# Kernel optimization log

Hardware: AMD Instinct MI355X
Metric: run time of the kernel (lower is better)

The kernel has to match this reference:

```python
import jax, jax.numpy as jnp
import numpy as np

N, IN, HID, OUT, C, H = 50000, 1488, 1024, 512, 32, 8
E = 800000

def setup_inputs() -> dict:
    key = jax.random.key(0)
    ks = jax.random.split(key, 16)
    s = lambda k, shape, fan: jax.random.normal(k, shape, jnp.float32) * (1.0 / np.sqrt(fan))
    return {
        "x": jax.random.normal(ks[0], (N, IN), jnp.float32),
        "edge_index": jax.random.randint(ks[1], (2, E), 0, N, jnp.int64),
        "ln_g": jnp.ones((IN,), jnp.float32),
        "ln_b": jnp.zeros((IN,), jnp.float32),
        "W1": s(ks[2], (IN, HID), IN), "b1": jnp.zeros((HID,), jnp.float32),
        "W2": s(ks[3], (HID, OUT), HID), "b2": jnp.zeros((OUT,), jnp.float32),
        "Wr": s(ks[4], (OUT, C * H), OUT), "br": jnp.zeros((C * H,), jnp.float32),
        "Wg": s(ks[5], (OUT, C * H), OUT),
        "att_src": s(ks[6], (H, C), C),
        "att_dst": s(ks[7], (H, C), C),
        "bg": jnp.zeros((C * H,), jnp.float32),
    }

def reference(x, edge_index, ln_g, ln_b, W1, b1, W2, b2, Wr, br, Wg, att_src, att_dst, bg):
    n = x.shape[0]
    # LayerNorm
    mu = jnp.mean(x, axis=-1, keepdims=True)
    var = jnp.mean(jnp.square(x - mu), axis=-1, keepdims=True)
    xn = (x - mu) * jax.lax.rsqrt(var + 1e-5) * ln_g + ln_b
    # init_proj MLP
    h = jax.nn.relu(xn @ W1 + b1) @ W2 + b2            # [N, OUT]
    res = h @ Wr + br                                   # [N, H*C]
    # GATConv (add_self_loops=True, dropout inactive in eval)
    loops = jnp.arange(n, dtype=edge_index.dtype)
    src = jnp.concatenate([edge_index[0], loops])
    dst = jnp.concatenate([edge_index[1], loops])
    g = (h @ Wg).reshape(n, H, C)                       # [N, H, C]
    a_src = jnp.sum(g * att_src, axis=-1)               # [N, H]
    a_dst = jnp.sum(g * att_dst, axis=-1)               # [N, H]
    e = jax.nn.leaky_relu(a_src[src] + a_dst[dst], 0.2) # [E', H]
    m = jax.ops.segment_max(e, dst, num_segments=n)     # per-dst softmax (stable)
    ex = jnp.exp(e - m[dst])
    denom = jax.ops.segment_sum(ex, dst, num_segments=n)
    alpha = ex / (denom[dst] + 1e-16)                   # [E', H]
    msg = alpha[:, :, None] * g[src]                    # [E', H, C]
    agg = jax.ops.segment_sum(msg, dst, num_segments=n) # [N, H, C]
    out = agg.reshape(n, H * C) + bg
    return jax.nn.elu(out) + res
```

## Files before the change

kernel.cpp:

```cpp
#include <hip/hip_runtime.h>
#include <hip/hip_bf16.h>
#include <cstdint>
#include <cstddef>

#define NND 50000
#define DIN 1488
#define DINP 1536
#define DHID 1024
#define DOUT 512
#define DHC 256
#define NE 800000
#define NHD 8
#define SPLITC 256

typedef __attribute__((ext_vector_type(8))) short short8;
typedef __attribute__((ext_vector_type(4))) short short4v;
typedef __attribute__((ext_vector_type(4))) float f32x4;
typedef __attribute__((ext_vector_type(4))) int int4v;
typedef unsigned short ushort_t;

__device__ __forceinline__ unsigned short f2bf(float f){
  union { float f; unsigned u; } v; v.f = f;
  unsigned r = v.u + 0x7fffu + ((v.u >> 16) & 1u);
  return (unsigned short)(r >> 16);
}
__device__ __forceinline__ float bf2f(unsigned short u){
  union { unsigned u; float f; } v; v.u = ((unsigned)u) << 16;
  return v.f;
}

__device__ __forceinline__ void async16(const void* g, void* l){
  __builtin_amdgcn_global_load_lds((__attribute__((address_space(1))) void*)g,
                                   (__attribute__((address_space(3))) void*)l, 16, 0, 0);
}

__device__ __forceinline__ void tc_tile(const float* __restrict__ W,
                                        ushort_t* __restrict__ WT,
                                        int K, int Nn, int Kp, int bx, int by){
  __shared__ float tile[32][33];
  const int tx = threadIdx.x & 31, ty = threadIdx.x >> 5;
  const int k0 = bx*32, n0 = by*32;
  for (int i = ty; i < 32; i += 8){
    int k = k0 + i, n = n0 + tx;
    tile[i][tx] = (k < K && n < Nn) ? W[(size_t)k*Nn + n] : 0.f;
  }
  __syncthreads();
  for (int i = ty; i < 32; i += 8){
    int n = n0 + i, k = k0 + tx;
    if (n < Nn && k < Kp) WT[(size_t)n*Kp + k] = f2bf(tile[tx][i]);
  }
}
__global__ __launch_bounds__(256) void prep_kernel(const float* W1, const float* W2,
                                                   const float* Wr, const float* Wg,
                                                   ushort_t* W1T, ushort_t* W2T,
                                                   ushort_t* WrgT, int* cnt){
  int b = blockIdx.x;
  if (b < 1536){ tc_tile(W1, W1T, DIN, DHID, DINP, b % 48, b / 48); return; }
  b -= 1536;
  if (b < 512){ tc_tile(W2, W2T, DHID, DOUT, DHID, b % 32, b / 32); return; }
  b -= 512;
  if (b < 128){ tc_tile(Wr, WrgT, DOUT, DHC, DOUT, b % 16, b / 16); return; }
  b -= 128;
  if (b < 128){ tc_tile(Wg, WrgT + 256*DOUT, DOUT, DHC, DOUT, b % 16, b / 16); return; }
  b -= 128;
  { int i = b*256 + threadIdx.x; if (i < NND) cnt[i] = 0; }
}

#define LN_BLOCKS 12500
__global__ __launch_bounds__(256) void ln_count(const float* __restrict__ x,
                                                const float* __restrict__ gw,
                                                const float* __restrict__ bw,
                                                ushort_t* __restrict__ xn,
                                                const int* __restrict__ ei,
                                                int* __restrict__ cnt){
  const int bid = blockIdx.x;
  if (bid >= LN_BLOCKS){
    int e = (bid - LN_BLOCKS)*256 + threadIdx.x;
    if (e < NE) atomicAdd(&cnt[ei[NE + e]], 1);
    return;
  }
  const int wid = threadIdx.x >> 6, lane = threadIdx.x & 63;
  const int row = bid*4 + wid;
  if (row >= NND) return;
  const float* xr = x + (size_t)row * DIN;
  float s = 0.f, sq = 0.f;
  for (int i = lane*4; i < DIN; i += 256){
    f32x4 v = *(const f32x4*)(xr + i);
    s  += v.x + v.y + v.z + v.w;
    sq += v.x*v.x + v.y*v.y + v.z*v.z + v.w*v.w;
  }
  #pragma unroll
  for (int o = 32; o; o >>= 1){ s += __shfl_xor(s, o); sq += __shfl_xor(sq, o); }
  const float mu = s * (1.f/DIN);
  const float var = sq * (1.f/DIN) - mu*mu;
  const float rstd = rsqrtf(var + 1e-5f);
  ushort_t* xo = xn + (size_t)row * DINP;
  for (int i = lane*4; i < DIN; i += 256){
    f32x4 v = *(const f32x4*)(xr + i);
    f32x4 gg = *(const f32x4*)(gw + i);
    f32x4 bb = *(const f32x4*)(bw + i);
    union { ushort_t u[4]; unsigned long long q; } o;
    o.u[0] = f2bf((v.x-mu)*rstd*gg.x + bb.x);
    o.u[1] = f2bf((v.y-mu)*rstd*gg.y + bb.y);
    o.u[2] = f2bf((v.z-mu)*rstd*gg.z + bb.z);
    o.u[3] = f2bf((v.w-mu)*rstd*gg.w + bb.w);
    *(unsigned long long*)(xo + i) = o.q;
  }
  if (lane < (DINP - DIN)) xo[DIN + lane] = 0;
}

#define G1_NWG 3128
template<int ACT, int MODE, int CB>
__global__ __launch_bounds__(256, 2) void gemm128(const ushort_t* __restrict__ A,
                                                  const ushort_t* __restrict__ BT,
                                                  const float* __restrict__ bias,
                                                  void* __restrict__ out0,
                                                  void* __restrict__ out1,
                                                  int M, int Nn, int K,
                                                  const int* __restrict__ cnt,
                                                  int* __restrict__ offs,
                                                  int* __restrict__ cur){
  __shared__ __align__(16) ushort_t lds[2][2][128*64];
  const int t = threadIdx.x, wid = t >> 6, lane = t & 63;

  if (blockIdx.x == 0){
    int* buf = (int*)&lds[0][0][0];
    const int chunk = (NND + 255) >> 8;
    const int s0 = t*chunk;
    const int s1 = (s0 + chunk < NND) ? s0 + chunk : NND;
    int s = 0;
    for (int i = s0; i < s1; i += 4){
      int4v v = *(const int4v*)(cnt + i);
      s += v.x + v.y + v.z + v.w + 4;
    }
    buf[t] = s; __syncthreads();
    for (int o = 1; o < 256; o <<= 1){
      int xv = (t >= o) ? buf[t-o] : 0;
      __syncthreads();
      buf[t] += xv;
      __syncthreads();
    }
    int run = buf[t] - s;
    for (int i = s0; i < s1; i += 4){
      int4v v = *(const int4v*)(cnt + i);
      int4v cu;
      cu.x = run; run += v.x + 1;
      cu.y = run; run += v.y + 1;
      cu.z = run; run += v.z + 1;
      cu.w = run; run += v.w + 1;
      *(int4v*)(cur + i)  = cu;
      *(int4v*)(offs + i) = cu;
    }
    if (t == 255) offs[NND] = run;
    return;
  }

  const int bid = blockIdx.x - 1, nwg = G1_NWG;
  const int q = nwg >> 3, r = nwg & 7;
  const int xcd = bid & 7, slot = bid >> 3;
  const int lg = (xcd < r ? xcd*(q+1) : r*(q+1) + (xcd - r)*q) + slot;
  const int brow = (lg / CB) * 128, bcol = (lg % CB) * 128;

  const int l8  = t >> 3;
  const int cb  = (t & 7) << 4;
  const int scb = cb ^ ((l8 & 7) << 4);
  const ushort_t* pAr[4]; const ushort_t* pBr[4];
  #pragma unroll
  for (int rd = 0; rd < 4; ++rd){
    int ra = brow + rd*32 + l8; ra = ra < M ? ra : M-1;
    int rb = bcol + rd*32 + l8; rb = rb < Nn ? rb : Nn-1;
    pAr[rd] = A  + (size_t)ra*K + (scb >> 1);
    pBr[rd] = BT + (size_t)rb*K + (scb >> 1);
  }
  const int w8 = wid * 8;

#define STAGE1(buf, kt) do {                                           \
    const int _o = (kt) * 64;                                          \
    _Pragma("unroll")                                                  \
    for (int _rd = 0; _rd < 4; ++_rd){                                 \
      async16(pAr[_rd] + _o, &lds[buf][0][(_rd*32 + w8)*64]);          \
      async16(pBr[_rd] + _o, &lds[buf][1][(_rd*32 + w8)*64]);          \
    }                                                                  \
  } while(0)

  f32x4 acc[4][4];
  #pragma unroll
  for (int i=0;i<4;i++)
    #pragma unroll
    for (int j=0;j<4;j++) acc[i][j] = (f32x4){0.f,0.f,0.f,0.f};

  const int wr = (wid >> 1)*64, wc = (wid & 1)*64;
  const int fr = lane & 15;
  const int kb0 = (lane >> 4) << 4;
  const int sx  = (fr & 7) << 4;
  const int ko0 = ((kb0      ) ^ sx) >> 1;
  const int ko1 = ((kb0 | 64 ) ^ sx) >> 1;

  const int nk = K >> 6;
  STAGE1(0, 0);
  STAGE1(1, 1);
  for (int kt = 0; kt < nk; ++kt){
    const ushort_t* bA = lds[kt & 1][0];
    const ushort_t* bB = lds[kt & 1][1];
    if (kt + 1 < nk) asm volatile("s_waitcnt vmcnt(8)" ::: "memory");
    else             asm volatile("s_waitcnt vmcnt(0)" ::: "memory");
    __builtin_amdgcn_s_barrier();
    short8 af[4][2], bf_[4][2];
    #pragma unroll
    for (int m=0;m<4;m++){
      const int ra = (wr + m*16 + fr)*64;
      const int rb = (wc + m*16 + fr)*64;
      af[m][0]  = *(const short8*)&bA[ra + ko0];
      af[m][1]  = *(const short8*)&bA[ra + ko1];
      bf_[m][0] = *(const short8*)&bB[rb + ko0];
      bf_[m][1] = *(const short8*)&bB[rb + ko1];
    }
    asm volatile("s_waitcnt lgkmcnt(0)" ::: "memory");
    __builtin_amdgcn_sched_barrier(0);
    __builtin_amdgcn_s_barrier();
    if (kt + 2 < nk) STAGE1(kt & 1, kt + 2);
    __builtin_amdgcn_s_setprio(1);
    #pragma unroll
    for (int m=0;m<4;m++)
      #pragma unroll
      for (int n=0;n<4;n++){
        acc[m][n] = __builtin_amdgcn_mfma_f32_16x16x32_bf16(af[m][0], bf_[n][0], acc[m][n], 0, 0, 0);
        acc[m][n] = __builtin_amdgcn_mfma_f32_16x16x32_bf16(af[m][1], bf_[n][1], acc[m][n], 0, 0, 0);
      }
    __builtin_amdgcn_s_setprio(0);
  }
#undef STAGE1

  bool isf32;
  float* outF = nullptr; ushort_t* outB = nullptr; int ostride = 0, ocb = 0;
  if (MODE == 0){ isf32 = true;  outF = (float*)out0;    ostride = Nn; ocb = bcol; }
  else if (MODE == 1){ isf32 = false; outB = (ushort_t*)out0; ostride = Nn; ocb = bcol; }
  else {
    if (bcol < SPLITC){ isf32 = true;  outF = (float*)out0;    ostride = SPLITC;      ocb = bcol; }
    else              { isf32 = false; outB = (ushort_t*)out1; ostride = Nn - SPLITC; ocb = bcol - SPLITC; }
  }
  float bv[4];
  #pragma unroll
  for (int n=0;n<4;n++){
    const int col = wc + n*16 + (lane & 15);
    float b = 0.f;
    if (MODE == 2){ if (isf32 && bias) b = bias[bcol + col]; }
    else if (bias) b = bias[bcol + col];
    bv[n] = b;
  }
  float* sF = (float*)&lds[0][0][0];
  ushort_t* sB = (ushort_t*)&lds[0][0][0];
  const int trow = t >> 3, tc16 = (t & 7) * 16;
  #pragma unroll
  for (int c = 0; c < 4; ++c){
    __syncthreads();
    if ((wid >> 1) == (c >> 1)){
      #pragma unroll
      for (int mm = 0; mm < 2; ++mm){
        const int m = 2*(c & 1) + mm;
        const int rbase = m*16 + (lane >> 4)*4 - (c & 1)*32;
        #pragma unroll
        for (int n = 0; n < 4; ++n){
          const int col = wc + n*16 + (lane & 15);
          #pragma unroll
          for (int j = 0; j < 4; ++j){
            float v = acc[m][n][j] + bv[n];
            if (ACT) v = v > 0.f ? v : 0.f;
            if (isf32) sF[(rbase + j)*128 + col] = v;
            else       sB[(rbase + j)*128 + col] = f2bf(v);
          }
        }
      }
    }
    __syncthreads();
    const int grow = brow + c*32 + trow;
    if (grow < M){
      if (isf32){
        float* dst = outF + (size_t)grow*ostride + ocb + tc16;
        const float* src = sF + trow*128 + tc16;
        #pragma unroll
        for (int q2 = 0; q2 < 4; ++q2) ((f32x4*)dst)[q2] = ((const f32x4*)src)[q2];
      } else {
        ushort_t* dst = outB + (size_t)grow*ostride + ocb + tc16;
        const ushort_t* src = sB + trow*128 + tc16;
        #pragma unroll
        for (int q2 = 0; q2 < 2; ++q2) ((short8*)dst)[q2] = ((const short8*)src)[q2];
      }
    }
  }
}

#define G2_NWG 392
template<int ACT, int MODE, int CB, int EXTRA>
__global__ __launch_bounds__(512, 2) void gemm256(const ushort_t* __restrict__ A,
                                                  const ushort_t* __restrict__ BT,
                                                  const float* __restrict__ bias,
                                                  void* __restrict__ out0,
                                                  void* __restrict__ out1,
                                                  int M, int Nn, int K,
                                                  const int* __restrict__ ei,
                                                  int* __restrict__ cur,
                                                  int* __restrict__ eidx,
                                                  const float* __restrict__ att_s,
                                                  const float* __restrict__ att_d,
                                                  float* __restrict__ asrc,
                                                  float* __restrict__ adst){
  __shared__ __align__(16) ushort_t lds[2][2][256*64];
  const int t = threadIdx.x, wid = t >> 6, lane = t & 63;

  if (EXTRA == 1 && blockIdx.x >= G2_NWG){
    int i = (blockIdx.x - G2_NWG)*512 + t;
    if (i < NND){
      int p = atomicAdd(&cur[i], 1); eidx[p] = i;
    } else if (i < NND + NE){
      int e = i - NND;
      int src = ei[e], dst = ei[NE + e];
      int p = atomicAdd(&cur[dst], 1);
      eidx[p] = src;
    }
    return;
  }

  const int bid = blockIdx.x, nwg = G2_NWG;
  const int q = nwg >> 3, r = nwg & 7;
  const int xcd = bid & 7, slot = bid >> 3;
  const int lg = (xcd < r ? xcd*(q+1) : r*(q+1) + (xcd - r)*q) + slot;
  const int brow = (lg / CB) * 256, bcol = (lg % CB) * 256;

  const int l8  = t >> 3;
  const int cb  = (t & 7) << 4;
  const unsigned scb = (unsigned)(cb ^ ((l8 & 7) << 4));
  unsigned rowA[4], rowB[4];
  #pragma unroll
  for (int rd = 0; rd < 4; ++rd){
    int ra = brow + rd*64 + l8; ra = ra < M ? ra : M-1;
    int rb = bcol + rd*64 + l8; rb = rb < Nn ? rb : Nn-1;
    rowA[rd] = (unsigned)ra * (unsigned)(K*2);
    rowB[rd] = (unsigned)rb * (unsigned)(K*2);
  }
  const int wst = (wid * 8) * 64;

#define STAGE2(buf, kt) do {                                              \
    const unsigned _ob = (unsigned)(kt)*128u + scb;                       \
    _Pragma("unroll")                                                     \
    for (int _rd = 0; _rd < 4; ++_rd){                                    \
      async16((const char*)A  + rowA[_rd] + _ob, &lds[buf][0][_rd*64*64 + wst]); \
      async16((const char*)BT + rowB[_rd] + _ob, &lds[buf][1][_rd*64*64 + wst]); \
    }                                                                     \
  } while(0)

  f32x4 acc[8][4];
  #pragma unroll
  for (int i=0;i<8;i++)
    #pragma unroll
    for (int j=0;j<4;j++) acc[i][j] = (f32x4){0.f,0.f,0.f,0.f};

  const int wrow = (wid >> 2), wcol = (wid & 3);
  const int fr = lane & 15;
  const int kb0 = (lane >> 4) << 4;
  const int sx  = (fr & 7) << 4;
  const int ko0 = ((kb0      ) ^ sx) >> 1;
  const int ko1 = ((kb0 | 64 ) ^ sx) >> 1;

  const int nk = K >> 6;
  STAGE2(0, 0);
  STAGE2(1, 1);
  for (int kt = 0; kt < nk; ++kt){
    const ushort_t* bA = lds[kt & 1][0];
    const ushort_t* bB = lds[kt & 1][1];
    if (kt + 1 < nk) asm volatile("s_waitcnt vmcnt(8)" ::: "memory");
    else             asm volatile("s_waitcnt vmcnt(0)" ::: "memory");
    __builtin_amdgcn_s_barrier();
    short8 af[8][2], bf_[4][2];
    #pragma unroll
    for (int m=0;m<8;m++){
      const int ra = (wrow*128 + m*16 + fr)*64;
      af[m][0] = *(const short8*)&bA[ra + ko0];
      af[m][1] = *(const short8*)&bA[ra + ko1];
    }
    #pragma unroll
    for (int n=0;n<4;n++){
      const int rb = (wcol*64 + n*16 + fr)*64;
      bf_[n][0] = *(const short8*)&bB[rb + ko0];
      bf_[n][1] = *(const short8*)&bB[rb + ko1];
    }
    asm volatile("s_waitcnt lgkmcnt(0)" ::: "memory");
    __builtin_amdgcn_sched_barrier(0);
    __builtin_amdgcn_s_barrier();
    if (kt + 2 < nk) STAGE2(kt & 1, kt + 2);
    __builtin_amdgcn_s_setprio(1);
    #pragma unroll
    for (int m=0;m<8;m++)
      #pragma unroll
      for (int n=0;n<4;n++){
        acc[m][n] = __builtin_amdgcn_mfma_f32_16x16x32_bf16(af[m][0], bf_[n][0], acc[m][n], 0, 0, 0);
        acc[m][n] = __builtin_amdgcn_mfma_f32_16x16x32_bf16(af[m][1], bf_[n][1], acc[m][n], 0, 0, 0);
      }
    __builtin_amdgcn_s_setprio(0);
  }
#undef STAGE2

  const bool isf32 = (MODE == 0) || (MODE == 2 && bcol == 0);
  float bv[4];
  #pragma unroll
  for (int n=0;n<4;n++){
    const int col = bcol + wcol*64 + n*16 + (lane & 15);
    float b = 0.f;
    if (MODE == 1){ if (bias) b = bias[col]; }
    if (MODE == 2){ if (isf32) b = bias[col]; }
    bv[n] = b;
  }

  if (isf32){
    float* outF; int ostride, ocb;
    if (MODE == 0){ outF = (float*)out0; ostride = Nn;  ocb = bcol; }
    else          { outF = (float*)out0; ostride = 256; ocb = 0;    }
    float* sF = (float*)&lds[0][0][0];
    #pragma unroll
    for (int p = 0; p < 2; ++p){
      __syncthreads();
      if (wrow == p){
        #pragma unroll
        for (int m=0;m<8;m++){
          const int row = m*16 + (lane >> 4)*4;
          #pragma unroll
          for (int n=0;n<4;n++){
            const int col = wcol*64 + n*16 + (lane & 15);
            #pragma unroll
            for (int j=0;j<4;j++){
              float v = acc[m][n][j] + bv[n];
              if (ACT) v = v > 0.f ? v : 0.f;
              sF[(row+j)*256 + col] = v;
            }
          }
        }
      }
      __syncthreads();
      const int srow = t >> 6, scol4 = (t & 63) * 4;
      #pragma unroll
      for (int rr = 0; rr < 16; ++rr){
        const int rloc = rr*8 + srow;
        const int grow = brow + p*128 + rloc;
        if (grow < M)
          *(f32x4*)(outF + (size_t)grow*ostride + ocb + scol4) = *(const f32x4*)&sF[rloc*256 + scol4];
      }
    }
  } else {
    ushort_t* outB; int ostride, ocb;
    if (MODE == 1){ outB = (ushort_t*)out0; ostride = Nn;  ocb = bcol; }
    else          { outB = (ushort_t*)out1; ostride = 256; ocb = 0;    }
    ushort_t* sB = (ushort_t*)&lds[0][0][0];
    __syncthreads();
    #pragma unroll
    for (int m=0;m<8;m++){
      const int row = wrow*128 + m*16 + (lane >> 4)*4;
      #pragma unroll
      for (int n=0;n<4;n++){
        const int col = wcol*64 + n*16 + (lane & 15);
        #pragma unroll
        for (int j=0;j<4;j++){
          float v = acc[m][n][j] + bv[n];
          if (ACT) v = v > 0.f ? v : 0.f;
          sB[(row+j)*256 + col] = f2bf(v);
        }
      }
    }
    __syncthreads();
    const int srow = t >> 5, scol8 = (t & 31) * 8;
    #pragma unroll
    for (int rr = 0; rr < 16; ++rr){
      const int rloc = rr*16 + srow;
      const int grow = brow + rloc;
      if (grow < M)
        *(short8*)(outB + (size_t)grow*ostride + ocb + scol8) = *(const short8*)&sB[rloc*256 + scol8];
    }
    if (MODE == 2){
      const int h = t & 7;
      const int hc0 = h * 32;
      #pragma unroll
      for (int k = 0; k < 4; ++k){
        const int rloc = (t >> 3) + k*64;
        const int grow = brow + rloc;
        if (grow < M){
          float a = 0.f, d = 0.f;
          #pragma unroll
          for (int c0 = 0; c0 < 32; c0 += 8){
            short8 gv = *(const short8*)&sB[rloc*256 + hc0 + c0];
            #pragma unroll
            for (int j = 0; j < 8; ++j){
              float g = bf2f((ushort_t)gv[j]);
              a += g*att_s[hc0 + c0 + j];
              d += g*att_d[hc0 + c0 + j];
            }
          }
          asrc[grow*NHD + h] = a;
          adst[grow*NHD + h] = d;
        }
      }
    }
  }
}

__global__ __launch_bounds__(256) void gat_agg(const int* __restrict__ offs,
                                               const int* __restrict__ eidx,
                                               const float* __restrict__ asrc,
                                               const float* __restrict__ adst,
                                               const ushort_t* __restrict__ gm,
                                               const float* __restrict__ res,
                                               const float* __restrict__ bg,
                                               float* __restrict__ out){
  const int wid = threadIdx.x >> 6, lane = threadIdx.x & 63;
  const int node = blockIdx.x*4 + wid;
  if (node >= NND) return;
  const int h = lane >> 3, jj = lane & 7;
  const int e0 = offs[node], deg = offs[node+1] - e0;
  const float adv = adst[node*NHD + h];

  float mx = -1e30f;
  for (int j = jj; j < deg; j += 8){
    int s = eidx[e0 + j];
    float e = asrc[s*NHD + h] + adv; e = e > 0.f ? e : 0.2f*e;
    mx = fmaxf(mx, e);
  }
  mx = fmaxf(mx, __shfl_xor(mx, 1));
  mx = fmaxf(mx, __shfl_xor(mx, 2));
  mx = fmaxf(mx, __shfl_xor(mx, 4));

  const int c4 = lane*4;
  float sm = 0.f;
  f32x4 acc = {0.f,0.f,0.f,0.f};
  for (int j0 = 0; j0 < deg; j0 += 8){
    const int cnt = (deg - j0) < 8 ? (deg - j0) : 8;
    int s = 0; float w = 0.f;
    if (jj < cnt){
      s = eidx[e0 + j0 + jj];
      float e = asrc[s*NHD + h] + adv; e = e > 0.f ? e : 0.2f*e;
      w = __expf(e - mx);
      sm += w;
    }
    #pragma unroll
    for (int u = 0; u < 8; ++u){
      if (u < cnt){
        const int   su = __builtin_amdgcn_readlane(s, u);
        const float wu = __shfl(w, (h << 3) | u);
        short4v gv = *(const short4v*)(gm + (size_t)su*DHC + c4);
        acc.x += wu*bf2f((ushort_t)gv.x);
        acc.y += wu*bf2f((ushort_t)gv.y);
        acc.z += wu*bf2f((ushort_t)gv.z);
        acc.w += wu*bf2f((ushort_t)gv.w);
      }
    }
  }
  sm += __shfl_xor(sm, 1); sm += __shfl_xor(sm, 2); sm += __shfl_xor(sm, 4);
  const float inv = 1.f/(sm + 1e-16f);

  f32x4 bgv = *(const f32x4*)(bg + c4);
  f32x4 rv  = *(const f32x4*)(res + (size_t)node*DHC + c4);
  f32x4 o;
  #pragma unroll
  for (int q = 0; q < 4; ++q){
    float v = acc[q]*inv + bgv[q];
    v = v > 0.f ? v : expm1f(v);
    o[q] = v + rv[q];
  }
  *(f32x4*)(out + (size_t)node*DHC + c4) = o;
}

extern "C" void kernel_launch(void* const* d_in, const int* in_sizes, int n_in,
                              void* d_out, int out_size, void* d_ws, size_t ws_size,
                              hipStream_t stream){
  (void)in_sizes; (void)n_in; (void)out_size; (void)ws_size;
  const float* x     = (const float*)d_in[0];
  const int*   ei    = (const int*)d_in[1];
  const float* ln_g  = (const float*)d_in[2];
  const float* ln_b  = (const float*)d_in[3];
  const float* W1    = (const float*)d_in[4];
  const float* b1    = (const float*)d_in[5];
  const float* W2    = (const float*)d_in[6];
  const float* b2    = (const float*)d_in[7];
  const float* Wr    = (const float*)d_in[8];
  const float* br    = (const float*)d_in[9];
  const float* Wg    = (const float*)d_in[10];
  const float* att_s = (const float*)d_in[11];
  const float* att_d = (const float*)d_in[12];
  const float* bg    = (const float*)d_in[13];
  float* out = (float*)d_out;

  char* p = (char*)d_ws;
  ushort_t* xn   = (ushort_t*)(p);
  ushort_t* h1   = (ushort_t*)(p + 153600000);
  float*    asrc = (float*)(p + 256000000);
  float*    adst = (float*)(p + 257600000);
  int*      cnt  = (int*)(p + 259200000);
  int*      offs = (int*)(p + 259400064);
  int*      cur  = (int*)(p + 259600128);
  int*      eidx = (int*)(p + 259800192);
  ushort_t* W1T  = (ushort_t*)d_out;
  ushort_t* W2T  = (ushort_t*)((char*)d_out + 3145728);
  ushort_t* WrgT = (ushort_t*)((char*)d_out + 4194304);
  ushort_t* hb   = (ushort_t*)(p + 0);
  float*    res  = (float*)(p + 51200000);
  ushort_t* gm   = (ushort_t*)(p + 102400000);

  prep_kernel<<<2500, 256, 0, stream>>>(W1, W2, Wr, Wg, W1T, W2T, WrgT, cnt);

  ln_count<<<LN_BLOCKS + (NE + 255)/256, 256, 0, stream>>>(x, ln_g, ln_b, xn, ei, cnt);

  gemm128<1,1,8><<<G1_NWG + 1, 256, 0, stream>>>(xn, W1T, b1, h1, nullptr,
                                                 NND, DHID, DINP, cnt, offs, cur);

  gemm256<0,1,2,1><<<G2_NWG + (NND + NE + 511)/512, 512, 0, stream>>>(
      h1, W2T, b2, hb, nullptr, NND, DOUT, DHID,
      ei, cur, eidx, nullptr, nullptr, nullptr, nullptr);

  gemm256<0,2,2,0><<<G2_NWG, 512, 0, stream>>>(
      hb, WrgT, br, res, gm, NND, 2*DHC, DOUT,
      nullptr, nullptr, nullptr, att_s, att_d, asrc, adst);

  gat_agg<<<(NND + 3)/4, 256, 0, stream>>>(offs, eidx, asrc, adst, gm, res, bg, out);
}
```

Baseline: 575.9 us.

## Fold W2 into Wr/Wg by precomputing combined weight and bias

Precomputes Wc = W2·[Wr|Wg] (512x1024 in bf16) and a folded bias b2·[Wr|Wg]+br on device. The separate h = h1·W2 GEMM is dropped, and the second GEMM now reads h1 directly with K=1024. This removes one full N×512 GEMM plus its intermediate write and read. In exchange the second GEMM does twice the K-work, and the combined weight is rounded to bf16 after the product, which slightly changes numerics.

```diff
diff --git a/kernel.cpp b/kernel.cpp
--- a/kernel.cpp
+++ b/kernel.cpp
@@ -50,19 +50,44 @@
     if (n < Nn && k < Kp) WT[(size_t)n*Kp + k] = f2bf(tile[tx][i]);
   }
 }
-__global__ __launch_bounds__(256) void prep_kernel(const float* W1, const float* W2,
-                                                   const float* Wr, const float* Wg,
-                                                   ushort_t* W1T, ushort_t* W2T,
-                                                   ushort_t* WrgT, int* cnt){
+__global__ __launch_bounds__(256) void prep_kernel(const float* W1, const float* Wr,
+                                                   const float* Wg, const float* W2,
+                                                   const float* b2, const float* br,
+                                                   ushort_t* W1T, ushort_t* WrgT,
+                                                   ushort_t* W2bf, float* b2rg,
+                                                   int* cnt){
   int b = blockIdx.x;
   if (b < 1536){ tc_tile(W1, W1T, DIN, DHID, DINP, b % 48, b / 48); return; }
   b -= 1536;
-  if (b < 512){ tc_tile(W2, W2T, DHID, DOUT, DHID, b % 32, b / 32); return; }
-  b -= 512;
   if (b < 128){ tc_tile(Wr, WrgT, DOUT, DHC, DOUT, b % 16, b / 16); return; }
   b -= 128;
   if (b < 128){ tc_tile(Wg, WrgT + 256*DOUT, DOUT, DHC, DOUT, b % 16, b / 16); return; }
   b -= 128;
+  if (b < 256){
+    const int idx = (b*256 + threadIdx.x)*8;
+    f32x4 v0 = *(const f32x4*)(W2 + idx);
+    f32x4 v1 = *(const f32x4*)(W2 + idx + 4);
+    union { ushort_t u[8]; short8 s; } o;
+    o.u[0]=f2bf(v0.x); o.u[1]=f2bf(v0.y); o.u[2]=f2bf(v0.z); o.u[3]=f2bf(v0.w);
+    o.u[4]=f2bf(v1.x); o.u[5]=f2bf(v1.y); o.u[6]=f2bf(v1.z); o.u[7]=f2bf(v1.w);
+    *(short8*)(W2bf + idx) = o.s;
+    return;
+  }
+  b -= 256;
+  if (b < 2){
+    const int c = b*256 + threadIdx.x;
+    float acc = 0.f;
+    if (c < 256){
+      for (int j = 0; j < DOUT; ++j) acc += b2[j]*Wr[(size_t)j*DHC + c];
+      acc += br[c];
+    } else {
+      const int cc = c - 256;
+      for (int j = 0; j < DOUT; ++j) acc += b2[j]*Wg[(size_t)j*DHC + cc];
+    }
+    b2rg[c] = acc;
+    return;
+  }
+  b -= 2;
   { int i = b*256 + threadIdx.x; if (i < NND) cnt[i] = 0; }
 }
 
@@ -109,8 +134,7 @@
   if (lane < (DINP - DIN)) xo[DIN + lane] = 0;
 }
 
-#define G1_NWG 3128
-template<int ACT, int MODE, int CB>
+template<int ACT, int MODE, int CB, int SCAN>
 __global__ __launch_bounds__(256, 2) void gemm128(const ushort_t* __restrict__ A,
                                                   const ushort_t* __restrict__ BT,
                                                   const float* __restrict__ bias,
@@ -123,7 +147,7 @@
   __shared__ __align__(16) ushort_t lds[2][2][128*64];
   const int t = threadIdx.x, wid = t >> 6, lane = t & 63;
 
-  if (blockIdx.x == 0){
+  if (SCAN == 1 && blockIdx.x == 0){
     int* buf = (int*)&lds[0][0][0];
     const int chunk = (NND + 255) >> 8;
     const int s0 = t*chunk;
@@ -155,7 +179,7 @@
     return;
   }
 
-  const int bid = blockIdx.x - 1, nwg = G1_NWG;
+  const int bid = blockIdx.x - SCAN, nwg = gridDim.x - SCAN;
   const int q = nwg >> 3, r = nwg & 7;
   const int xcd = bid & 7, slot = bid >> 3;
   const int lg = (xcd < r ? xcd*(q+1) : r*(q+1) + (xcd - r)*q) + slot;
@@ -407,7 +431,7 @@
     const int col = bcol + wcol*64 + n*16 + (lane & 15);
     float b = 0.f;
     if (MODE == 1){ if (bias) b = bias[col]; }
-    if (MODE == 2){ if (isf32) b = bias[col]; }
+    if (MODE == 2){ b = bias[col]; }
     bv[n] = b;
   }
 
@@ -596,26 +620,27 @@
   int*      cur  = (int*)(p + 259600128);
   int*      eidx = (int*)(p + 259800192);
   ushort_t* W1T  = (ushort_t*)d_out;
-  ushort_t* W2T  = (ushort_t*)((char*)d_out + 3145728);
-  ushort_t* WrgT = (ushort_t*)((char*)d_out + 4194304);
-  ushort_t* hb   = (ushort_t*)(p + 0);
-  float*    res  = (float*)(p + 51200000);
-  ushort_t* gm   = (ushort_t*)(p + 102400000);
-
-  prep_kernel<<<2500, 256, 0, stream>>>(W1, W2, Wr, Wg, W1T, W2T, WrgT, cnt);
+  ushort_t* WrgT = (ushort_t*)((char*)d_out + 3145728);
+  ushort_t* W2bf = (ushort_t*)((char*)d_out + 3670016);
+  ushort_t* WcT  = (ushort_t*)((char*)d_out + 4718592);
+  float*    b2rg = (float*)((char*)d_out + 5767168);
+  float*    res  = (float*)(p + 0);
+  ushort_t* gm   = (ushort_t*)(p + 51200000);
+
+  prep_kernel<<<2246, 256, 0, stream>>>(W1, Wr, Wg, W2, b2, br,
+                                        W1T, WrgT, W2bf, b2rg, cnt);
+
+  gemm128<0,1,8,0><<<32, 256, 0, stream>>>(WrgT, W2bf, nullptr, WcT, nullptr,
+                                           512, 1024, 512, nullptr, nullptr, nullptr);
 
   ln_count<<<LN_BLOCKS + (NE + 255)/256, 256, 0, stream>>>(x, ln_g, ln_b, xn, ei, cnt);
 
-  gemm128<1,1,8><<<G1_NWG + 1, 256, 0, stream>>>(xn, W1T, b1, h1, nullptr,
+  gemm128<1,1,8,1><<<3128 + 1, 256, 0, stream>>>(xn, W1T, b1, h1, nullptr,
                                                  NND, DHID, DINP, cnt, offs, cur);
 
-  gemm256<0,1,2,1><<<G2_NWG + (NND + NE + 511)/512, 512, 0, stream>>>(
-      h1, W2T, b2, hb, nullptr, NND, DOUT, DHID,
-      ei, cur, eidx, nullptr, nullptr, nullptr, nullptr);
-
-  gemm256<0,2,2,0><<<G2_NWG, 512, 0, stream>>>(
-      hb, WrgT, br, res, gm, NND, 2*DHC, DOUT,
-      nullptr, nullptr, nullptr, att_s, att_d, asrc, adst);
+  gemm256<0,2,2,1><<<G2_NWG + (NND + NE + 511)/512, 512, 0, stream>>>(
+      h1, WcT, b2rg, res, gm, NND, 2*DHC, DHID,
+      ei, cur, eidx, att_s, att_d, asrc, adst);
 
   gat_agg<<<(NND + 3)/4, 256, 0, stream>>>(offs, eidx, asrc, adst, gm, res, bg, out);
 }
```

After: 551.4 us. -4.3%, faster.
